# Performance work log

Measured on AMD Instinct MI355X. Metric: run time of the kernel, lower is better.

Reference implementation:

```python
import jax, jax.numpy as jnp
import numpy as np
import math

SR = 44100
FRAME = 256
K = 80
NB = 16
MIDI_LO, MIDI_HI = 21.0, 108.0


def setup_inputs() -> dict:
    key = jax.random.key(0)
    k0, k1 = jax.random.split(key)
    B = 8
    # fundamental frequencies spread over ~4 octaves of the piano range (55..880 Hz)
    f0 = 55.0 * 2.0 ** (jax.random.uniform(k0, (B,)) * 4.0)
    vel_norm = jax.random.uniform(k1, (B,), minval=0.2, maxval=1.0)
    inp = dict(
        f0=f0.astype(jnp.float32),
        vel_norm=vel_norm.astype(jnp.float32),
        log_B_slope=jnp.float32(-2.0),
        log_B_intercept=jnp.float32(-7.5),
        log_tau1=jnp.linspace(math.log(0.4), math.log(0.05), K).astype(jnp.float32),
        log_tau2=jnp.linspace(math.log(5.0), math.log(0.3), K).astype(jnp.float32),
        logit_a1=jnp.linspace(-1.4, 0.0, K).astype(jnp.float32),
        log_beat_hz=jnp.linspace(math.log(0.3), math.log(1.5), K).astype(jnp.float32),
        logit_beat_depth=jnp.full((K,), -1.7, jnp.float32),
        log_A0=(-jnp.log(jnp.arange(1, K + 1, dtype=jnp.float32)) * 0.7),
        harm_detune=jnp.zeros((K,), jnp.float32),
        noise_band_gain=jnp.zeros((NB,), jnp.float32),
        log_tau_noise=jnp.float32(math.log(0.05)),
        log_noise_level=jnp.float32(math.log(0.08)),
        pan_scale=jnp.float32(0.0),
        n_frames=256,
    )
    return inp


def reference(f0, vel_norm, log_B_slope, log_B_intercept, log_tau1, log_tau2,
              logit_a1, log_beat_hz, logit_beat_depth, log_A0, harm_detune,
              noise_band_gain, log_tau_noise, log_noise_level, pan_scale,
              n_frames):
    N = n_frames * FRAME                                   # total audio samples
    t = jnp.arange(N, dtype=jnp.float32) * jnp.float32(1.0 / SR)   # (N,)
    two_pi = jnp.float32(2.0 * math.pi)

    # --- inharmonicity coefficient B(midi) = exp(clamp(slope*m + intercept)) ---
    midi = 69.0 + 12.0 * jnp.log2(f0 / 440.0)
    midi_norm = (midi - MIDI_LO) / (MIDI_HI - MIDI_LO)
    B_inh = jnp.exp(jnp.clip(log_B_slope * midi_norm + log_B_intercept, -14.0, -4.0))  # (B,)

    # --- inharmonic partial frequencies f_k = f0 * k * sqrt(1 + B k^2) ---
    ks = jnp.arange(1, K + 1, dtype=jnp.float32)           # (K,)
    freqs = f0[:, None] * ks * jnp.sqrt(1.0 + B_inh[:, None] * ks ** 2)  # (B,K)
    freqs = freqs * (1.0 + harm_detune)                    # learned per-partial detune
    alive = (freqs < SR / 2).astype(jnp.float32)           # nyquist mask (B,K)

    # --- double-exponential decay envelope per partial ---
    tau1 = jnp.exp(log_tau1)
    tau2 = jnp.exp(log_tau2)
    a1 = jax.nn.sigmoid(logit_a1)
    env = (a1[:, None] * jnp.exp(-t / tau1[:, None])
           + (1.0 - a1[:, None]) * jnp.exp(-t / tau2[:, None]))        # (K,N)

    # --- beating modulation (two-string coupling) ---
    depth = jax.nn.sigmoid(logit_beat_depth)
    bhz = jnp.exp(log_beat_hz)
    beat = 1.0 + 0.5 * depth[:, None] * (jnp.cos(two_pi * bhz[:, None] * t) - 1.0)  # (K,N)

    # --- oscillator bank: amp * env * beat * sin(2 pi f t) ---
    amp = jnp.exp(log_A0)[None, :] * vel_norm[:, None] * alive          # (B,K)
    phase = two_pi * freqs[:, :, None] * t                              # (B,K,N)
    partials = (amp[:, :, None] * (env * beat)[None]) * jnp.sin(phase)  # (B,K,N)

    # --- stereo panning per partial (constant-power) ---
    pan_init = (jnp.arange(K, dtype=jnp.float32) / max(K - 1, 1) * 2.0 - 1.0) * 0.1
    pan = jnp.tanh(pan_init * jnp.exp(pan_scale))                       # (K,)
    gains = jnp.stack([jnp.sqrt(0.5 * (1.0 - pan)),
                       jnp.sqrt(0.5 * (1.0 + pan))])                    # (2,K)
    audio = jnp.einsum('bkn,ck->bcn', partials, gains)                  # (B,2,N)

    # --- attack noise: log-spaced band oscillators with fast exp decay ---
    nf = jnp.exp(jnp.linspace(math.log(200.0), math.log(20000.0), NB)).astype(jnp.float32)
    n_alive = (nf < SR / 2).astype(jnp.float32)
    band_g = jax.nn.softmax(noise_band_gain) * n_alive                  # (NB,)
    noise_osc = jnp.sin(two_pi * nf[:, None] * t)                       # (NB,N)
    noise_env = jnp.exp(-t / jnp.exp(log_tau_noise))                    # (N,)
    noise_sig = (band_g @ noise_osc) * noise_env                        # (N,)
    noise = jnp.exp(log_noise_level) * vel_norm[:, None] * noise_sig[None, :]  # (B,N)

    return audio + noise[:, None, :]                                    # (B,2,N)
```

## Files before the change

kernel.cpp:

```cpp
#include <hip/hip_runtime.h>
#include <math.h>


#define KMAX 128
#define NBMAX 32


__device__ __forceinline__ float sin_acc(float ph) {
    double d = (double)ph;
    double q = rint(d * 1.5915494309189535e-01);
    double r = fma(q, -6.283185307179586, d);
    return __sinf((float)r);
}

__global__ void pr_precomp(const float* __restrict__ f0,
                           const float* __restrict__ vel,
                           const float* __restrict__ pslope,
                           const float* __restrict__ pinter,
                           const float* __restrict__ log_tau1,
                           const float* __restrict__ log_tau2,
                           const float* __restrict__ logit_a1,
                           const float* __restrict__ log_beat_hz,
                           const float* __restrict__ logit_beat_depth,
                           const float* __restrict__ log_A0,
                           const float* __restrict__ harm_detune,
                           const float* __restrict__ noise_band_gain,
                           const float* __restrict__ plog_tau_noise,
                           const float* __restrict__ plog_noise_level,
                           const float* __restrict__ ppan_scale,
                           float* __restrict__ ws, int B, int K, int NB) {
    const int tid = threadIdx.x;
    const float two_pi = (float)(2.0 * 3.14159265358979323846);
    const float slope = pslope[0], inter = pinter[0], pan_scale = ppan_scale[0];

    float* pf  = ws;
    float* cL  = ws + (size_t)B * K;
    float* cR  = ws + (size_t)2 * B * K;
    float* it1 = ws + (size_t)3 * B * K;
    float* it2 = it1 + K;
    float* a1s = it2 + K;
    float* om1 = a1s + K;
    float* wb  = om1 + K;
    float* hd  = wb + K;
    float* bg  = hd + K;
    float* wn  = bg + NB;
    float* nl  = wn + NB;
    float* itn = nl + B;

    for (int i = tid; i < B * K; i += blockDim.x) {
        int b = i / K, k = i % K;
        float f0b = f0[b];
        float kf = (float)(k + 1);
        float midi = 69.0f + 12.0f * log2f(f0b / 440.0f);
        float mn = (midi - 21.0f) / 87.0f;
        float z = slope * mn + inter;
        z = fminf(fmaxf(z, -14.0f), -4.0f);
        float Binh = expf(z);
        float freq = (f0b * kf) * sqrtf(1.0f + Binh * (kf * kf));
        freq = freq * (1.0f + harm_detune[k]);
        float alive = (freq < 22050.0f) ? 1.0f : 0.0f;
        float amp = expf(log_A0[k]) * vel[b] * alive;
        int km1 = (K - 1) > 1 ? (K - 1) : 1;
        float pini = ((float)k / (float)km1 * 2.0f - 1.0f) * 0.1f;
        float pan = tanhf(pini * expf(pan_scale));
        float gl = sqrtf(0.5f * (1.0f - pan));
        float gr = sqrtf(0.5f * (1.0f + pan));
        pf[i] = two_pi * freq;
        cL[i] = amp * gl;
        cR[i] = amp * gr;
    }
    for (int k = tid; k < K; k += blockDim.x) {
        it1[k] = 1.0f / expf(log_tau1[k]);
        it2[k] = 1.0f / expf(log_tau2[k]);
        float a1 = 1.0f / (1.0f + expf(-logit_a1[k]));
        a1s[k] = a1;
        om1[k] = 1.0f - a1;
        wb[k] = two_pi * expf(log_beat_hz[k]);
        hd[k] = 0.5f * (1.0f / (1.0f + expf(-logit_beat_depth[k])));
    }
    for (int j = tid; j < NB; j += blockDim.x) {
        float m = -1e30f;
        for (int q = 0; q < NB; ++q) m = fmaxf(m, noise_band_gain[q]);
        float ssum = 0.0f;
        for (int q = 0; q < NB; ++q) ssum += expf(noise_band_gain[q] - m);
        float start = logf(200.0f), stop = logf(20000.0f);
        float step = (stop - start) / (float)(NB - 1);
        float lin = (j == NB - 1) ? stop : (start + (float)j * step);
        float nf = expf(lin);
        float na = (nf < 22050.0f) ? 1.0f : 0.0f;
        bg[j] = (expf(noise_band_gain[j] - m) / ssum) * na;
        wn[j] = two_pi * nf;
    }
    for (int b = tid; b < B; b += blockDim.x)
        nl[b] = expf(plog_noise_level[0]) * vel[b];
    if (tid == 0) itn[0] = 1.0f / expf(plog_tau_noise[0]);
}

__global__ __launch_bounds__(256) void pr_synth(const float* __restrict__ ws,
                                                float* __restrict__ out,
                                                int B, int K, int NB, int N) {
    const float* pf  = ws;
    const float* cL  = ws + (size_t)B * K;
    const float* cR  = ws + (size_t)2 * B * K;
    const float* it1 = ws + (size_t)3 * B * K;
    const float* it2 = it1 + K;
    const float* a1s = it2 + K;
    const float* om1 = a1s + K;
    const float* wb  = om1 + K;
    const float* hd  = wb + K;
    const float* bg  = hd + K;
    const float* wn  = bg + NB;
    const float* nl  = wn + NB;
    const float* itn = nl + B;

    const int b = blockIdx.y;
    const int n = blockIdx.x * blockDim.x + threadIdx.x;

    __shared__ float s_pf[KMAX], s_cL[KMAX], s_cR[KMAX];
    __shared__ float s_it1[KMAX], s_it2[KMAX], s_a1[KMAX], s_om[KMAX];
    __shared__ float s_wb[KMAX], s_hd[KMAX];
    __shared__ float s_bg[NBMAX], s_wn[NBMAX];

    for (int i = threadIdx.x; i < K; i += blockDim.x) {
        s_pf[i]  = pf[(size_t)b * K + i];
        s_cL[i]  = cL[(size_t)b * K + i];
        s_cR[i]  = cR[(size_t)b * K + i];
        s_it1[i] = it1[i];
        s_it2[i] = it2[i];
        s_a1[i]  = a1s[i];
        s_om[i]  = om1[i];
        s_wb[i]  = wb[i];
        s_hd[i]  = hd[i];
    }
    for (int i = threadIdx.x; i < NB; i += blockDim.x) {
        s_bg[i] = bg[i];
        s_wn[i] = wn[i];
    }
    __syncthreads();
    if (n >= N) return;

    const float t = (float)n * (float)(1.0 / 44100.0);

    float accL = 0.0f, accR = 0.0f;
    for (int k = 0; k < K; ++k) {
        float cl = s_cL[k], cr = s_cR[k];
        if (cl == 0.0f && cr == 0.0f) continue;
        float e1 = __expf(-t * s_it1[k]);
        float e2 = __expf(-t * s_it2[k]);
        float env = s_a1[k] * e1 + s_om[k] * e2;
        float beat = fmaf(s_hd[k], __cosf(s_wb[k] * t) - 1.0f, 1.0f);
        float eb = env * beat;
        float sv = sin_acc(s_pf[k] * t);
        float p = eb * sv;
        accL = fmaf(cl, p, accL);
        accR = fmaf(cr, p, accR);
    }

    float ns = 0.0f;
    for (int j = 0; j < NB; ++j)
        ns = fmaf(s_bg[j], sin_acc(s_wn[j] * t), ns);
    float nenv = __expf(-t * itn[0]);
    float nois = nl[b] * (ns * nenv);

    out[((size_t)b * 2 + 0) * N + n] = accL + nois;
    out[((size_t)b * 2 + 1) * N + n] = accR + nois;
}

extern "C" void kernel_launch(void* const* d_in, const int* in_sizes, int n_in,
                              void* d_out, int out_size, void* d_ws, size_t ws_size,
                              hipStream_t stream) {
    const float* f0    = (const float*)d_in[0];
    const float* vel   = (const float*)d_in[1];
    const float* slope = (const float*)d_in[2];
    const float* inter = (const float*)d_in[3];
    const float* lt1   = (const float*)d_in[4];
    const float* lt2   = (const float*)d_in[5];
    const float* la1   = (const float*)d_in[6];
    const float* lbh   = (const float*)d_in[7];
    const float* lbd   = (const float*)d_in[8];
    const float* lA0   = (const float*)d_in[9];
    const float* hdet  = (const float*)d_in[10];
    const float* nbg   = (const float*)d_in[11];
    const float* ltn   = (const float*)d_in[12];
    const float* lnl   = (const float*)d_in[13];
    const float* pans  = (const float*)d_in[14];

    const int B  = in_sizes[0];
    const int K  = in_sizes[4];
    const int NB = in_sizes[11];
    const int N  = out_size / (2 * B);

    float* ws = (float*)d_ws;

    hipLaunchKernelGGL(pr_precomp, dim3(1), dim3(256), 0, stream,
                       f0, vel, slope, inter, lt1, lt2, la1, lbh, lbd, lA0,
                       hdet, nbg, ltn, lnl, pans, ws, B, K, NB);

    dim3 grid((N + 255) / 256, B);
    hipLaunchKernelGGL(pr_synth, grid, dim3(256), 0, stream,
                       ws, (float*)d_out, B, K, NB, N);
}
```

Baseline: 127.3 us.

## Share per-partial envelope across batch tile and use float Cody-Waite sine reduction

The synth kernel now handles 8 batch items per thread. The envelope exps and beat cosine, which do not depend on the batch item, are computed once per partial and reused for all 8 items. The double-precision range reduction for sine is replaced by a two-constant float Cody-Waite reduction, which removes costly FP64 ops in the inner loop. Partial parameters are packed into float4 for shared-memory loads, and the precompute moves to double-precision math with no-fuse barriers to track reference rounding. In exchange, the zero-amplitude skip is dropped, and the grid becomes small (N/128 x 1 blocks of 128 threads), which may reduce occupancy.

```diff
diff --git a/kernel.cpp b/kernel.cpp
--- a/kernel.cpp
+++ b/kernel.cpp
@@ -5,13 +5,22 @@
 #define KMAX 128
 #define NBMAX 32
 
-
-__device__ __forceinline__ float sin_acc(float ph) {
-    double d = (double)ph;
-    double q = rint(d * 1.5915494309189535e-01);
-    double r = fma(q, -6.283185307179586, d);
-    return __sinf((float)r);
-}
+#define C2PI_HI 6.28318548202514648f
+#define C2PI_LO -1.7484556e-7f
+#define INV2PI  0.15915494309189535f
+
+__device__ __forceinline__ float nofuse(float x) {
+    asm volatile("" : "+v"(x));
+    return x;
+}
+
+__device__ __forceinline__ float sin_cw(float ph) {
+    float q = rintf(ph * INV2PI);
+    float r = fmaf(q, -C2PI_HI, ph);
+    r = fmaf(q, -C2PI_LO, r);
+    return __sinf(r);
+}
+
 
 __global__ void pr_precomp(const float* __restrict__ f0,
                            const float* __restrict__ vel,
@@ -30,140 +39,151 @@
                            const float* __restrict__ ppan_scale,
                            float* __restrict__ ws, int B, int K, int NB) {
     const int tid = threadIdx.x;
-    const float two_pi = (float)(2.0 * 3.14159265358979323846);
+    const float two_pi = C2PI_HI;
     const float slope = pslope[0], inter = pinter[0], pan_scale = ppan_scale[0];
 
-    float* pf  = ws;
-    float* cL  = ws + (size_t)B * K;
-    float* cR  = ws + (size_t)2 * B * K;
-    float* it1 = ws + (size_t)3 * B * K;
-    float* it2 = it1 + K;
-    float* a1s = it2 + K;
-    float* om1 = a1s + K;
-    float* wb  = om1 + K;
-    float* hd  = wb + K;
-    float* bg  = hd + K;
-    float* wn  = bg + NB;
-    float* nl  = wn + NB;
-    float* itn = nl + B;
+    float4* pk4 = (float4*)ws;
+    float4* keA = pk4 + (size_t)B * K;
+    float4* keB = keA + K;
+    float4* nz  = keB + K;
+    float*  nl  = (float*)(nz + NB);
 
     for (int i = tid; i < B * K; i += blockDim.x) {
         int b = i / K, k = i % K;
         float f0b = f0[b];
         float kf = (float)(k + 1);
-        float midi = 69.0f + 12.0f * log2f(f0b / 440.0f);
+        float fr = f0b / 440.0f;
+        float midi = 69.0f + 12.0f * (float)log2((double)fr);
         float mn = (midi - 21.0f) / 87.0f;
-        float z = slope * mn + inter;
+        float z = nofuse(slope * mn) + inter;
         z = fminf(fmaxf(z, -14.0f), -4.0f);
-        float Binh = expf(z);
-        float freq = (f0b * kf) * sqrtf(1.0f + Binh * (kf * kf));
-        freq = freq * (1.0f + harm_detune[k]);
-        float alive = (freq < 22050.0f) ? 1.0f : 0.0f;
-        float amp = expf(log_A0[k]) * vel[b] * alive;
+        float Binh = (float)exp((double)z);
+        float kk  = kf * kf;
+        float bk2 = nofuse(Binh * kk);
+        float arg = nofuse(1.0f + bk2);
+        float s3  = (float)sqrt((double)arg);
+        float r0  = nofuse(f0b * kf);
+        float r1  = nofuse(r0 * s3);
+        float dt  = nofuse(1.0f + harm_detune[k]);
+        float fq  = nofuse(r1 * dt);
+        float alive = (fq < 22050.0f) ? 1.0f : 0.0f;
+        float amp = (float)exp((double)log_A0[k]) * vel[b] * alive;
         int km1 = (K - 1) > 1 ? (K - 1) : 1;
-        float pini = ((float)k / (float)km1 * 2.0f - 1.0f) * 0.1f;
-        float pan = tanhf(pini * expf(pan_scale));
-        float gl = sqrtf(0.5f * (1.0f - pan));
-        float gr = sqrtf(0.5f * (1.0f + pan));
-        pf[i] = two_pi * freq;
-        cL[i] = amp * gl;
-        cR[i] = amp * gr;
+        float a = (float)k / (float)km1;
+        float pini = nofuse((a * 2.0f - 1.0f) * 0.1f);
+        float pexp = (float)exp((double)pan_scale);
+        float pan = (float)tanh((double)nofuse(pini * pexp));
+        float gl = (float)sqrt((double)(0.5f * (1.0f - pan)));
+        float gr = (float)sqrt((double)(0.5f * (1.0f + pan)));
+        float pf = nofuse(two_pi * fq);
+        pk4[i] = make_float4(pf, amp * gl, amp * gr, 0.0f);
     }
     for (int k = tid; k < K; k += blockDim.x) {
-        it1[k] = 1.0f / expf(log_tau1[k]);
-        it2[k] = 1.0f / expf(log_tau2[k]);
-        float a1 = 1.0f / (1.0f + expf(-logit_a1[k]));
-        a1s[k] = a1;
-        om1[k] = 1.0f - a1;
-        wb[k] = two_pi * expf(log_beat_hz[k]);
-        hd[k] = 0.5f * (1.0f / (1.0f + expf(-logit_beat_depth[k])));
+        float tau1 = (float)exp((double)log_tau1[k]);
+        float tau2 = (float)exp((double)log_tau2[k]);
+        float a1 = (float)(1.0 / (1.0 + exp(-(double)logit_a1[k])));
+        float bhz = (float)exp((double)log_beat_hz[k]);
+        float dep = (float)(1.0 / (1.0 + exp(-(double)logit_beat_depth[k])));
+        keA[k] = make_float4(1.0f / tau1, 1.0f / tau2, a1, 1.0f - a1);
+        keB[k] = make_float4(nofuse(two_pi * bhz), 0.5f * dep, 0.0f, 0.0f);
     }
     for (int j = tid; j < NB; j += blockDim.x) {
         float m = -1e30f;
         for (int q = 0; q < NB; ++q) m = fmaxf(m, noise_band_gain[q]);
         float ssum = 0.0f;
-        for (int q = 0; q < NB; ++q) ssum += expf(noise_band_gain[q] - m);
-        float start = logf(200.0f), stop = logf(20000.0f);
-        float step = (stop - start) / (float)(NB - 1);
-        float lin = (j == NB - 1) ? stop : (start + (float)j * step);
-        float nf = expf(lin);
+        for (int q = 0; q < NB; ++q)
+            ssum += (float)exp((double)(noise_band_gain[q] - m));
+        double start = log(200.0), stop = log(20000.0);
+        double step = (stop - start) / (double)(NB - 1);
+        float lin = (j == NB - 1) ? (float)stop : (float)(start + (double)j * step);
+        float nf = (float)exp((double)lin);
         float na = (nf < 22050.0f) ? 1.0f : 0.0f;
-        bg[j] = (expf(noise_band_gain[j] - m) / ssum) * na;
-        wn[j] = two_pi * nf;
+        float bg = ((float)exp((double)(noise_band_gain[j] - m)) / ssum) * na;
+        nz[j] = make_float4(nofuse(two_pi * nf), bg, 0.0f, 0.0f);
     }
     for (int b = tid; b < B; b += blockDim.x)
-        nl[b] = expf(plog_noise_level[0]) * vel[b];
-    if (tid == 0) itn[0] = 1.0f / expf(plog_tau_noise[0]);
-}
-
-__global__ __launch_bounds__(256) void pr_synth(const float* __restrict__ ws,
-                                                float* __restrict__ out,
-                                                int B, int K, int NB, int N) {
-    const float* pf  = ws;
-    const float* cL  = ws + (size_t)B * K;
-    const float* cR  = ws + (size_t)2 * B * K;
-    const float* it1 = ws + (size_t)3 * B * K;
-    const float* it2 = it1 + K;
-    const float* a1s = it2 + K;
-    const float* om1 = a1s + K;
-    const float* wb  = om1 + K;
-    const float* hd  = wb + K;
-    const float* bg  = hd + K;
-    const float* wn  = bg + NB;
-    const float* nl  = wn + NB;
-    const float* itn = nl + B;
-
-    const int b = blockIdx.y;
-    const int n = blockIdx.x * blockDim.x + threadIdx.x;
-
-    __shared__ float s_pf[KMAX], s_cL[KMAX], s_cR[KMAX];
-    __shared__ float s_it1[KMAX], s_it2[KMAX], s_a1[KMAX], s_om[KMAX];
-    __shared__ float s_wb[KMAX], s_hd[KMAX];
-    __shared__ float s_bg[NBMAX], s_wn[NBMAX];
-
-    for (int i = threadIdx.x; i < K; i += blockDim.x) {
-        s_pf[i]  = pf[(size_t)b * K + i];
-        s_cL[i]  = cL[(size_t)b * K + i];
-        s_cR[i]  = cR[(size_t)b * K + i];
-        s_it1[i] = it1[i];
-        s_it2[i] = it2[i];
-        s_a1[i]  = a1s[i];
-        s_om[i]  = om1[i];
-        s_wb[i]  = wb[i];
-        s_hd[i]  = hd[i];
-    }
-    for (int i = threadIdx.x; i < NB; i += blockDim.x) {
-        s_bg[i] = bg[i];
-        s_wn[i] = wn[i];
-    }
+        nl[b] = (float)exp((double)plog_noise_level[0]) * vel[b];
+    if (tid == 0) nl[B] = 1.0f / (float)exp((double)plog_tau_noise[0]);
+}
+
+template <int BT>
+__global__ __launch_bounds__(128) void pr_synth(
+    const float4* __restrict__ pk4, const float4* __restrict__ keA,
+    const float4* __restrict__ keB, const float4* __restrict__ nz,
+    const float* __restrict__ nlp, float* __restrict__ out,
+    int B, int K, int NB, int N) {
+    __shared__ float4 s_pk[BT * KMAX];
+    __shared__ float4 s_keA[KMAX];
+    __shared__ float4 s_keB[KMAX];
+    __shared__ float4 s_nz[NBMAX];
+    __shared__ float  s_nl[BT];
+    __shared__ float  s_itn;
+
+    const int tid = threadIdx.x;
+    const int bOff = blockIdx.y * BT;
+
+    for (int i = tid; i < BT * K; i += blockDim.x) {
+        int bi = i / K, k = i - bi * K;
+        int b = bOff + bi;
+        s_pk[i] = (b < B) ? pk4[(size_t)b * K + k] : make_float4(0, 0, 0, 0);
+    }
+    for (int i = tid; i < K; i += blockDim.x) {
+        s_keA[i] = keA[i];
+        s_keB[i] = keB[i];
+    }
+    for (int i = tid; i < NB; i += blockDim.x) s_nz[i] = nz[i];
+    for (int i = tid; i < BT; i += blockDim.x)
+        s_nl[i] = (bOff + i < B) ? nlp[bOff + i] : 0.0f;
+    if (tid == 0) s_itn = nlp[B];
     __syncthreads();
+
+    const int n = blockIdx.x * blockDim.x + tid;
     if (n >= N) return;
-
     const float t = (float)n * (float)(1.0 / 44100.0);
-
-    float accL = 0.0f, accR = 0.0f;
+    const float nt = -t;
+
+    float accL[BT], accR[BT];
+#pragma unroll
+    for (int bi = 0; bi < BT; ++bi) { accL[bi] = 0.0f; accR[bi] = 0.0f; }
+
     for (int k = 0; k < K; ++k) {
-        float cl = s_cL[k], cr = s_cR[k];
-        if (cl == 0.0f && cr == 0.0f) continue;
-        float e1 = __expf(-t * s_it1[k]);
-        float e2 = __expf(-t * s_it2[k]);
-        float env = s_a1[k] * e1 + s_om[k] * e2;
-        float beat = fmaf(s_hd[k], __cosf(s_wb[k] * t) - 1.0f, 1.0f);
+        float4 ka = s_keA[k];
+        float4 kb = s_keB[k];
+        float e1 = __expf(nt * ka.x);
+        float e2 = __expf(nt * ka.y);
+        float env = ka.z * e1 + ka.w * e2;
+        float beat = fmaf(kb.y, __cosf(kb.x * t) - 1.0f, 1.0f);
         float eb = env * beat;
-        float sv = sin_acc(s_pf[k] * t);
-        float p = eb * sv;
-        accL = fmaf(cl, p, accL);
-        accR = fmaf(cr, p, accR);
+#pragma unroll
+        for (int bi = 0; bi < BT; ++bi) {
+            float4 p = s_pk[bi * K + k];
+            float ph = p.x * t;
+            float q = rintf(ph * INV2PI);
+            float r = fmaf(q, -C2PI_HI, ph);
+            r = fmaf(q, -C2PI_LO, r);
+            float sv = __sinf(r);
+            float pp = eb * sv;
+            accL[bi] = fmaf(p.y, pp, accL[bi]);
+            accR[bi] = fmaf(p.z, pp, accR[bi]);
+        }
     }
 
     float ns = 0.0f;
-    for (int j = 0; j < NB; ++j)
-        ns = fmaf(s_bg[j], sin_acc(s_wn[j] * t), ns);
-    float nenv = __expf(-t * itn[0]);
-    float nois = nl[b] * (ns * nenv);
-
-    out[((size_t)b * 2 + 0) * N + n] = accL + nois;
-    out[((size_t)b * 2 + 1) * N + n] = accR + nois;
+    for (int j = 0; j < NB; ++j) {
+        float4 zj = s_nz[j];
+        ns = fmaf(zj.y, sin_cw(zj.x * t), ns);
+    }
+    float nsv = ns * __expf(nt * s_itn);
+
+#pragma unroll
+    for (int bi = 0; bi < BT; ++bi) {
+        int b = bOff + bi;
+        if (b < B) {
+            float nois = s_nl[bi] * nsv;
+            out[((size_t)(b * 2 + 0)) * N + n] = accL[bi] + nois;
+            out[((size_t)(b * 2 + 1)) * N + n] = accR[bi] + nois;
+        }
+    }
 }
 
 extern "C" void kernel_launch(void* const* d_in, const int* in_sizes, int n_in,
@@ -196,7 +216,13 @@
                        f0, vel, slope, inter, lt1, lt2, la1, lbh, lbd, lA0,
                        hdet, nbg, ltn, lnl, pans, ws, B, K, NB);
 
-    dim3 grid((N + 255) / 256, B);
-    hipLaunchKernelGGL(pr_synth, grid, dim3(256), 0, stream,
-                       ws, (float*)d_out, B, K, NB, N);
-}
+    const float4* pk4 = (const float4*)ws;
+    const float4* keA = pk4 + (size_t)B * K;
+    const float4* keB = keA + K;
+    const float4* nz  = keB + K;
+    const float*  nlp = (const float*)(nz + NB);
+
+    dim3 grid((N + 127) / 128, (B + 7) / 8);
+    hipLaunchKernelGGL(pr_synth<8>, grid, dim3(128), 0, stream,
+                       pk4, keA, keB, nz, nlp, (float*)d_out, B, K, NB, N);
+}
```

Result: no change. 126.0 us (-1.0%).
